# Optimization experiments

Hardware: AMD Instinct MI355X
Metric: run time of the kernel (lower is better)

Reference implementation:

```python
import jax, jax.numpy as jnp
import numpy as np

N_NODES = 100000


def setup_inputs() -> dict:
    key = jax.random.key(0)
    k1, k2, k3 = jax.random.split(key, 3)
    x = jax.random.normal(k1, (N_NODES, 128), dtype=jnp.float32)
    edge_index = jax.random.randint(k2, (2, 500000), 0, N_NODES, dtype=jnp.int64)
    # GCNConv linear weight (glorot-ish scale) and bias
    W = jax.random.normal(k3, (128, 512), dtype=jnp.float32) * (1.0 / np.sqrt(128.0))
    b = jnp.zeros((512,), dtype=jnp.float32)
    prelu_w = jnp.full((512,), 0.25, dtype=jnp.float32)  # torch PReLU default init
    return {"x": x, "edge_index": edge_index, "W": W, "b": b, "prelu_w": prelu_w}


def reference(x, edge_index, W, b, prelu_w):
    N = x.shape[0]
    # 1) linear transform (GCNConv applies lin before aggregation, bias after)
    h = x @ W  # [N, H]
    # 2) add self-loops
    loops = jnp.arange(N, dtype=edge_index.dtype)
    src = jnp.concatenate([edge_index[0], loops])  # [E+N]
    dst = jnp.concatenate([edge_index[1], loops])
    # 3) symmetric normalization: deg computed on destination nodes
    deg = jax.ops.segment_sum(jnp.ones_like(src, dtype=h.dtype), dst, num_segments=N)
    dinv = jnp.where(deg > 0, deg ** -0.5, 0.0)
    norm = dinv[src] * dinv[dst]  # [E+N]
    # 4) normalized scatter-add aggregation
    msg = h[src] * norm[:, None]  # [E+N, H]
    out = jax.ops.segment_sum(msg, dst, num_segments=N) + b  # [N, H]
    # 5) channel-wise PReLU
    return jnp.where(out >= 0, out, prelu_w * out)
```

## Files before the change

### kernel.cpp

```cpp
#include <hip/hip_runtime.h>


typedef __attribute__((ext_vector_type(8))) short bf16x8_t;
typedef __attribute__((ext_vector_type(4))) float f32x4;

#define N_NODES 100000
#define N_EDGES 500000
#define K_IN    128
#define H_OUT   512
#define MAXDEG  32
#define NEB     1954
#define NMT     782

static __device__ __forceinline__ unsigned short f2b(float f) {
    unsigned u = __float_as_uint(f);
    u = (u + 0x7FFFu + ((u >> 16) & 1u)) >> 16;
    return (unsigned short)u;
}
static __device__ __forceinline__ float b2lo(unsigned v) {
    return __uint_as_float(v << 16);
}
static __device__ __forceinline__ float b2hi(unsigned v) {
    return __uint_as_float(v & 0xFFFF0000u);
}

__global__ __launch_bounds__(256) void k1(const int* __restrict__ ei,
                                          int* __restrict__ deg,
                                          int* __restrict__ csrp,
                                          const float* __restrict__ W,
                                          unsigned short* __restrict__ Wt) {
    int b = blockIdx.x;
    if (b < NEB) {
        int e = b * 256 + threadIdx.x;
        if (e < N_EDGES) {
            int s = ei[e];
            int d = ei[N_EDGES + e];
            int r = atomicAdd(&deg[d], 1);
            csrp[d * MAXDEG + r] = s;
        }
    } else {
        int i = (b - NEB) * 256 + threadIdx.x;
        int n = i >> 7, k = i & 127;
        Wt[i] = f2b(W[k * H_OUT + n]);
    }
}

__global__ __launch_bounds__(256) void k2(const int* __restrict__ deg,
                                          const float* __restrict__ x,
                                          unsigned* __restrict__ xs) {
    int i = blockIdx.x * 256 + threadIdx.x;
    int row = i >> 6;
    float d = rsqrtf((float)(deg[row] + 1));
    const float2* x2 = (const float2*)x;
    float2 xv = x2[i];
    xs[i] = ((unsigned)f2b(d * xv.y) << 16) | f2b(d * xv.x);
}

__global__ __launch_bounds__(256) void k5(const unsigned* __restrict__ xs,
                                          const int* __restrict__ csrp,
                                          const int* __restrict__ deg,
                                          unsigned* __restrict__ xa) {
    int wave = threadIdx.x >> 6, lane = threadIdx.x & 63;
    int node = blockIdx.x * 4 + wave;
    if (node >= N_NODES) return;

    unsigned sv = xs[(size_t)node * 64 + lane];
    int cnt = __builtin_amdgcn_readfirstlane(deg[node]);
    float a0 = b2lo(sv), a1 = b2hi(sv);

    const int4* cp = (const int4*)(csrp + node * MAXDEG);
    for (int j = 0; j < cnt; j += 8) {
        int4 ca = cp[(j >> 2)];
        int4 cb = cp[(j >> 2) + 1];
        unsigned idx[8] = {(unsigned)ca.x, (unsigned)ca.y, (unsigned)ca.z, (unsigned)ca.w,
                           (unsigned)cb.x, (unsigned)cb.y, (unsigned)cb.z, (unsigned)cb.w};
        unsigned v[8];
        #pragma unroll
        for (int t = 0; t < 8; ++t) {
            unsigned id = idx[t] < N_NODES ? idx[t] : 0u;
            v[t] = xs[(size_t)id * 64 + lane];
        }
        int rem = cnt - j;
        #pragma unroll
        for (int t = 0; t < 8; ++t) {
            unsigned val = (t < rem) ? v[t] : 0u;
            a0 += b2lo(val);
            a1 += b2hi(val);
        }
    }
    float di = rsqrtf((float)(cnt + 1));
    xa[(size_t)node * 64 + lane] = ((unsigned)f2b(di * a1) << 16) | f2b(di * a0);
}

__global__ __launch_bounds__(512) void k6(const unsigned short* __restrict__ xa,
                                          const unsigned short* __restrict__ Wt,
                                          const float* __restrict__ bias,
                                          const float* __restrict__ pw,
                                          float* __restrict__ out) {
    __shared__ char smem[65536];
    uint4* sA = (uint4*)smem;
    uint4* sB = (uint4*)(smem + 32768);
    float* ep = (float*)(smem + 32768);

    int orig = blockIdx.x;
    int xcd = orig & 7, loc = orig >> 3;
    int wgid = (xcd < 6 ? xcd * 98 : 588 + (xcd - 6) * 97) + loc;
    const int m0 = wgid * 128;
    const int tid = threadIdx.x;
    const int wave = tid >> 6, lane = tid & 63;

    const uint4* A4 = (const uint4*)xa;
    const uint4* B4 = (const uint4*)Wt;

    #pragma unroll
    for (int r = 0; r < 4; ++r) {
        int i = tid + r * 512;
        int row = i >> 4, c = i & 15;
        int grow = m0 + row;
        uint4 o = (grow < N_NODES) ? A4[(size_t)grow * 16 + c]
                                   : make_uint4(0u, 0u, 0u, 0u);
        sA[row * 16 + (c ^ (row & 7))] = o;
    }

    const int wr = wave >> 2, wc = wave & 3;
    const int l16 = lane & 15, lq = lane >> 4;

    for (int nc = 0; nc < 4; ++nc) {
        #pragma unroll
        for (int r = 0; r < 4; ++r) {
            int i = tid + r * 512;
            int row = i >> 4, c = i & 15;
            sB[row * 16 + (c ^ (row & 7))] = B4[(size_t)(nc * 128 + row) * 16 + c];
        }
        __syncthreads();

        f32x4 acc[4][2];
        #pragma unroll
        for (int m = 0; m < 4; ++m)
            #pragma unroll
            for (int n = 0; n < 2; ++n)
                acc[m][n] = (f32x4){0.f, 0.f, 0.f, 0.f};

        #pragma unroll
        for (int kk = 0; kk < 4; ++kk) {
            bf16x8_t av[4], bv[2];
            #pragma unroll
            for (int m = 0; m < 4; ++m) {
                int row = wr * 64 + m * 16 + l16;
                av[m] = __builtin_bit_cast(bf16x8_t, sA[row * 16 + ((kk * 4 + lq) ^ (row & 7))]);
            }
            #pragma unroll
            for (int n = 0; n < 2; ++n) {
                int row = wc * 32 + n * 16 + l16;
                bv[n] = __builtin_bit_cast(bf16x8_t, sB[row * 16 + ((kk * 4 + lq) ^ (row & 7))]);
            }
            #pragma unroll
            for (int m = 0; m < 4; ++m)
                #pragma unroll
                for (int n = 0; n < 2; ++n)
                    acc[m][n] = __builtin_amdgcn_mfma_f32_16x16x32_bf16(av[m], bv[n], acc[m][n], 0, 0, 0);
        }
        __syncthreads();

        float bn[2], pn[2];
        #pragma unroll
        for (int n = 0; n < 2; ++n) {
            int gn = nc * 128 + wc * 32 + n * 16 + l16;
            bn[n] = bias[gn];
            pn[n] = pw[gn];
        }

        #pragma unroll
        for (int h = 0; h < 2; ++h) {
            if (wr == h) {
                #pragma unroll
                for (int m = 0; m < 4; ++m)
                    #pragma unroll
                    for (int r = 0; r < 4; ++r) {
                        int row = m * 16 + lq * 4 + r;
                        #pragma unroll
                        for (int n = 0; n < 2; ++n) {
                            float t = acc[m][n][r] + bn[n];
                            float v = t >= 0.f ? t : pn[n] * t;
                            ep[row * 128 + wc * 32 + n * 16 + l16] = v;
                        }
                    }
            }
            __syncthreads();
            #pragma unroll
            for (int it = 0; it < 4; ++it) {
                int row = it * 16 + (tid >> 5);
                int gm = m0 + h * 64 + row;
                if (gm < N_NODES) {
                    int c4 = tid & 31;
                    f32x4 v = *(const f32x4*)&ep[row * 128 + c4 * 4];
                    __builtin_nontemporal_store(v, (f32x4*)&out[(size_t)gm * H_OUT + nc * 128 + c4 * 4]);
                }
            }
            __syncthreads();
        }
    }
}

extern "C" void kernel_launch(void* const* d_in, const int* in_sizes, int n_in,
                              void* d_out, int out_size, void* d_ws, size_t ws_size,
                              hipStream_t stream) {
    const float* x    = (const float*)d_in[0];
    const int*   ei   = (const int*)d_in[1];
    const float* W    = (const float*)d_in[2];
    const float* bias = (const float*)d_in[3];
    const float* pw   = (const float*)d_in[4];
    float* out = (float*)d_out;

    char* ws = (char*)d_ws;
    size_t off = 0;
    auto alloc = [&](size_t bytes) -> void* {
        void* p = ws + off;
        off += (bytes + 255) & ~(size_t)255;
        return p;
    };
    unsigned*       xs   = (unsigned*)alloc((size_t)N_NODES * K_IN * 2);
    unsigned*       xa   = (unsigned*)alloc((size_t)N_NODES * K_IN * 2);
    unsigned short* Wt   = (unsigned short*)alloc((size_t)K_IN * H_OUT * 2);
    int*            deg  = (int*)alloc((size_t)N_NODES * 4);
    int*            csrp = (int*)alloc((size_t)N_NODES * MAXDEG * 4);
    (void)ws_size; (void)in_sizes; (void)n_in; (void)out_size;

    hipMemsetAsync(deg, 0, (size_t)N_NODES * 4, stream);

    k1 <<<NEB + 256, 256, 0, stream>>>(ei, deg, csrp, W, Wt);
    k2 <<<25000, 256, 0, stream>>>(deg, x, xs);
    k5 <<<(N_NODES + 3) / 4, 256, 0, stream>>>(xs, csrp, deg, xa);
    k6 <<<NMT, 512, 0, stream>>>((const unsigned short*)xa,
                                 (const unsigned short*)Wt, bias, pw, out);
}
```

Measured before the change: 126.8 us.

## Gather neighbor features in fp8 and split self-loop term into separate bf16 buffer

The prescaled node features used for neighbor gathering are now stored as fp8 (4 bytes per 4 channels), halving gather traffic. Each wave handles two edges at once, one per half-wave, and the halves are combined with a cross-lane shuffle. The self-loop contribution is precomputed in bf16 with a dinv^2 scale and added at the end, so the node's own term keeps higher precision. Neighbor sums lose precision from the fp8 quantization, and k2 now writes two buffers.

```diff
diff --git a/kernel.cpp b/kernel.cpp
--- a/kernel.cpp
+++ b/kernel.cpp
@@ -3,6 +3,7 @@
 
 typedef __attribute__((ext_vector_type(8))) short bf16x8_t;
 typedef __attribute__((ext_vector_type(4))) float f32x4;
+typedef __attribute__((ext_vector_type(2))) float f32x2;
 
 #define N_NODES 100000
 #define N_EDGES 500000
@@ -47,49 +48,73 @@
 
 __global__ __launch_bounds__(256) void k2(const int* __restrict__ deg,
                                           const float* __restrict__ x,
-                                          unsigned* __restrict__ xs) {
+                                          unsigned* __restrict__ xsf,
+                                          unsigned* __restrict__ xai) {
     int i = blockIdx.x * 256 + threadIdx.x;
-    int row = i >> 6;
+    int row = i >> 5, c = i & 31;
     float d = rsqrtf((float)(deg[row] + 1));
-    const float2* x2 = (const float2*)x;
-    float2 xv = x2[i];
-    xs[i] = ((unsigned)f2b(d * xv.y) << 16) | f2b(d * xv.x);
-}
-
-__global__ __launch_bounds__(256) void k5(const unsigned* __restrict__ xs,
+    const float4* x4 = (const float4*)x;
+    float4 xv = x4[i];
+    int lo   = __builtin_amdgcn_cvt_pk_fp8_f32(d * xv.x, d * xv.y, 0, 0);
+    int both = __builtin_amdgcn_cvt_pk_fp8_f32(d * xv.z, d * xv.w, lo, 1);
+    xsf[i] = (unsigned)both;
+    float dd = d * d;
+    unsigned p0 = ((unsigned)f2b(dd * xv.y) << 16) | f2b(dd * xv.x);
+    unsigned p1 = ((unsigned)f2b(dd * xv.w) << 16) | f2b(dd * xv.z);
+    *(uint2*)&xai[(size_t)row * 64 + 2 * c] = make_uint2(p0, p1);
+}
+
+__global__ __launch_bounds__(256) void k5(const unsigned* __restrict__ xsf,
+                                          const unsigned* __restrict__ xai,
                                           const int* __restrict__ csrp,
                                           const int* __restrict__ deg,
                                           unsigned* __restrict__ xa) {
     int wave = threadIdx.x >> 6, lane = threadIdx.x & 63;
     int node = blockIdx.x * 4 + wave;
     if (node >= N_NODES) return;
-
-    unsigned sv = xs[(size_t)node * 64 + lane];
+    int l32 = lane & 31, hw = lane >> 5;
+
+    float a0 = 0.f, a1 = 0.f, a2 = 0.f, a3 = 0.f;
     int cnt = __builtin_amdgcn_readfirstlane(deg[node]);
-    float a0 = b2lo(sv), a1 = b2hi(sv);
-
     const int4* cp = (const int4*)(csrp + node * MAXDEG);
+
     for (int j = 0; j < cnt; j += 8) {
         int4 ca = cp[(j >> 2)];
         int4 cb = cp[(j >> 2) + 1];
         unsigned idx[8] = {(unsigned)ca.x, (unsigned)ca.y, (unsigned)ca.z, (unsigned)ca.w,
                            (unsigned)cb.x, (unsigned)cb.y, (unsigned)cb.z, (unsigned)cb.w};
-        unsigned v[8];
-        #pragma unroll
-        for (int t = 0; t < 8; ++t) {
-            unsigned id = idx[t] < N_NODES ? idx[t] : 0u;
-            v[t] = xs[(size_t)id * 64 + lane];
-        }
-        int rem = cnt - j;
-        #pragma unroll
-        for (int t = 0; t < 8; ++t) {
-            unsigned val = (t < rem) ? v[t] : 0u;
-            a0 += b2lo(val);
-            a1 += b2hi(val);
-        }
-    }
-    float di = rsqrtf((float)(cnt + 1));
-    xa[(size_t)node * 64 + lane] = ((unsigned)f2b(di * a1) << 16) | f2b(di * a0);
+        unsigned v[4];
+        #pragma unroll
+        for (int t = 0; t < 4; ++t) {
+            unsigned id = hw ? idx[2 * t + 1] : idx[2 * t];
+            id = id < N_NODES ? id : 0u;
+            v[t] = xsf[(size_t)id * 32 + l32];
+        }
+        #pragma unroll
+        for (int t = 0; t < 4; ++t) {
+            int e = j + 2 * t + hw;
+            unsigned val = (e < cnt) ? v[t] : 0u;
+            f32x2 p01 = __builtin_amdgcn_cvt_pk_f32_fp8((int)val, 0);
+            f32x2 p23 = __builtin_amdgcn_cvt_pk_f32_fp8((int)val, 1);
+            a0 += p01.x; a1 += p01.y; a2 += p23.x; a3 += p23.y;
+        }
+    }
+    a0 += __shfl_xor(a0, 32, 64);
+    a1 += __shfl_xor(a1, 32, 64);
+    a2 += __shfl_xor(a2, 32, 64);
+    a3 += __shfl_xor(a3, 32, 64);
+
+    if (hw == 0) {
+        float di = rsqrtf((float)(cnt + 1));
+        uint2 self = *(const uint2*)&xai[(size_t)node * 64 + 2 * l32];
+        float f0 = b2lo(self.x) + di * a0;
+        float f1 = b2hi(self.x) + di * a1;
+        float f2 = b2lo(self.y) + di * a2;
+        float f3 = b2hi(self.y) + di * a3;
+        unsigned d0 = ((unsigned)f2b(f1) << 16) | f2b(f0);
+        unsigned d1 = ((unsigned)f2b(f3) << 16) | f2b(f2);
+        *(uint2*)&xa[(size_t)node * 64 + 2 * l32] = make_uint2(d0, d1);
+    }
 }
 
 __global__ __launch_bounds__(512) void k6(const unsigned short* __restrict__ xa,
@@ -219,7 +244,8 @@
         off += (bytes + 255) & ~(size_t)255;
         return p;
     };
-    unsigned*       xs   = (unsigned*)alloc((size_t)N_NODES * K_IN * 2);
+    unsigned*       xsf  = (unsigned*)alloc((size_t)N_NODES * K_IN);
+    unsigned*       xai  = (unsigned*)alloc((size_t)N_NODES * K_IN * 2);
     unsigned*       xa   = (unsigned*)alloc((size_t)N_NODES * K_IN * 2);
     unsigned short* Wt   = (unsigned short*)alloc((size_t)K_IN * H_OUT * 2);
     int*            deg  = (int*)alloc((size_t)N_NODES * 4);
@@ -229,8 +255,8 @@
     hipMemsetAsync(deg, 0, (size_t)N_NODES * 4, stream);
 
     k1 <<<NEB + 256, 256, 0, stream>>>(ei, deg, csrp, W, Wt);
-    k2 <<<25000, 256, 0, stream>>>(deg, x, xs);
-    k5 <<<(N_NODES + 3) / 4, 256, 0, stream>>>(xs, csrp, deg, xa);
+    k2 <<<12500, 256, 0, stream>>>(deg, x, xsf, xai);
+    k5 <<<(N_NODES + 3) / 4, 256, 0, stream>>>(xsf, xai, csrp, deg, xa);
     k6 <<<NMT, 512, 0, stream>>>((const unsigned short*)xa,
                                  (const unsigned short*)Wt, bias, pw, out);
 }
```

Result: slower. 141.2 us (+11.4%).

## Fold x bf16 conversion into first kernel and apply source-degree scaling in gather

Applied to the files above, without the earlier changes.

The separate pass that scaled x by each node's inverse sqrt degree is removed. x is now converted to bf16 unscaled inside the edge/weight preprocessing launch, which gets extra blocks for this, and the aggregation kernel loads deg for each neighbour and applies the rsqrt weight during accumulation. This saves one kernel launch and a dependent full pass over x. The cost is an extra scattered degree load and an rsqrt per neighbour in the gather loop.

```diff
diff --git a/kernel.cpp b/kernel.cpp
--- a/kernel.cpp
+++ b/kernel.cpp
@@ -10,6 +10,8 @@
 #define H_OUT   512
 #define MAXDEG  32
 #define NEB     1954
+#define NWB     256
+#define NCB     12500
 #define NMT     782
 
 static __device__ __forceinline__ unsigned short f2b(float f) {
@@ -28,7 +30,9 @@
                                           int* __restrict__ deg,
                                           int* __restrict__ csrp,
                                           const float* __restrict__ W,
-                                          unsigned short* __restrict__ Wt) {
+                                          unsigned short* __restrict__ Wt,
+                                          const float* __restrict__ x,
+                                          unsigned* __restrict__ xraw) {
     int b = blockIdx.x;
     if (b < NEB) {
         int e = b * 256 + threadIdx.x;
@@ -38,25 +42,21 @@
             int r = atomicAdd(&deg[d], 1);
             csrp[d * MAXDEG + r] = s;
         }
-    } else {
+    } else if (b < NEB + NWB) {
         int i = (b - NEB) * 256 + threadIdx.x;
         int n = i >> 7, k = i & 127;
         Wt[i] = f2b(W[k * H_OUT + n]);
-    }
-}
-
-__global__ __launch_bounds__(256) void k2(const int* __restrict__ deg,
-                                          const float* __restrict__ x,
-                                          unsigned* __restrict__ xs) {
-    int i = blockIdx.x * 256 + threadIdx.x;
-    int row = i >> 6;
-    float d = rsqrtf((float)(deg[row] + 1));
-    const float2* x2 = (const float2*)x;
-    float2 xv = x2[i];
-    xs[i] = ((unsigned)f2b(d * xv.y) << 16) | f2b(d * xv.x);
-}
-
-__global__ __launch_bounds__(256) void k5(const unsigned* __restrict__ xs,
+    } else {
+        int t = (b - NEB - NWB) * 256 + threadIdx.x;
+        const float4* x4 = (const float4*)x;
+        float4 xv = x4[t];
+        unsigned p0 = ((unsigned)f2b(xv.y) << 16) | f2b(xv.x);
+        unsigned p1 = ((unsigned)f2b(xv.w) << 16) | f2b(xv.z);
+        *(uint2*)&xraw[2 * (size_t)t] = make_uint2(p0, p1);
+    }
+}
+
+__global__ __launch_bounds__(256) void k5(const unsigned* __restrict__ xraw,
                                           const int* __restrict__ csrp,
                                           const int* __restrict__ deg,
                                           unsigned* __restrict__ xa) {
@@ -64,9 +64,9 @@
     int node = blockIdx.x * 4 + wave;
     if (node >= N_NODES) return;
 
-    unsigned sv = xs[(size_t)node * 64 + lane];
+    unsigned sv = xraw[(size_t)node * 64 + lane];
     int cnt = __builtin_amdgcn_readfirstlane(deg[node]);
-    float a0 = b2lo(sv), a1 = b2hi(sv);
+    float a0 = 0.f, a1 = 0.f;
 
     const int4* cp = (const int4*)(csrp + node * MAXDEG);
     for (int j = 0; j < cnt; j += 8) {
@@ -75,21 +75,25 @@
         unsigned idx[8] = {(unsigned)ca.x, (unsigned)ca.y, (unsigned)ca.z, (unsigned)ca.w,
                            (unsigned)cb.x, (unsigned)cb.y, (unsigned)cb.z, (unsigned)cb.w};
         unsigned v[8];
+        int dg[8];
         #pragma unroll
         for (int t = 0; t < 8; ++t) {
             unsigned id = idx[t] < N_NODES ? idx[t] : 0u;
-            v[t] = xs[(size_t)id * 64 + lane];
+            v[t] = xraw[(size_t)id * 64 + lane];
+            dg[t] = deg[id];
         }
         int rem = cnt - j;
         #pragma unroll
         for (int t = 0; t < 8; ++t) {
-            unsigned val = (t < rem) ? v[t] : 0u;
-            a0 += b2lo(val);
-            a1 += b2hi(val);
+            float w = (t < rem) ? rsqrtf((float)(dg[t] + 1)) : 0.f;
+            a0 += w * b2lo(v[t]);
+            a1 += w * b2hi(v[t]);
         }
     }
     float di = rsqrtf((float)(cnt + 1));
-    xa[(size_t)node * 64 + lane] = ((unsigned)f2b(di * a1) << 16) | f2b(di * a0);
+    float f0 = di * (a0 + di * b2lo(sv));
+    float f1 = di * (a1 + di * b2hi(sv));
+    xa[(size_t)node * 64 + lane] = ((unsigned)f2b(f1) << 16) | f2b(f0);
 }
 
 __global__ __launch_bounds__(512) void k6(const unsigned short* __restrict__ xa,
@@ -219,7 +223,7 @@
         off += (bytes + 255) & ~(size_t)255;
         return p;
     };
-    unsigned*       xs   = (unsigned*)alloc((size_t)N_NODES * K_IN * 2);
+    unsigned*       xraw = (unsigned*)alloc((size_t)N_NODES * K_IN * 2);
     unsigned*       xa   = (unsigned*)alloc((size_t)N_NODES * K_IN * 2);
     unsigned short* Wt   = (unsigned short*)alloc((size_t)K_IN * H_OUT * 2);
     int*            deg  = (int*)alloc((size_t)N_NODES * 4);
@@ -228,9 +232,8 @@
 
     hipMemsetAsync(deg, 0, (size_t)N_NODES * 4, stream);
 
-    k1 <<<NEB + 256, 256, 0, stream>>>(ei, deg, csrp, W, Wt);
-    k2 <<<25000, 256, 0, stream>>>(deg, x, xs);
-    k5 <<<(N_NODES + 3) / 4, 256, 0, stream>>>(xs, csrp, deg, xa);
+    k1 <<<NEB + NWB + NCB, 256, 0, stream>>>(ei, deg, csrp, W, Wt, x, xraw);
+    k5 <<<(N_NODES + 3) / 4, 256, 0, stream>>>(xraw, csrp, deg, xa);
     k6 <<<NMT, 512, 0, stream>>>((const unsigned short*)xa,
                                  (const unsigned short*)Wt, bias, pw, out);
 }
```

New measurement: 127.6 us. No clear change (+0.7%).
